# Kernel optimization log

Measured on AMD Instinct MI355X. Metric: run time of the kernel, lower is better.

The kernel has to match this reference:

```python
import jax, jax.numpy as jnp
import numpy as np

N = 100000   # num_rows
M = 50000    # num_cols
D = 32       # embed_dim
E = 5000000  # num observed edges


def setup_inputs() -> dict:
    key = jax.random.key(0)
    ks = jax.random.split(key, 9)
    bound = 1.0 / np.sqrt(D)
    row_embed = jax.random.uniform(ks[0], (N, D), minval=-bound, maxval=bound, dtype=jnp.float32)
    col_embed = jax.random.uniform(ks[1], (M, D), minval=-bound, maxval=bound, dtype=jnp.float32)
    # kaiming_uniform_ with nonlinearity='relu': bound = sqrt(6 / fan_in)
    kb = np.sqrt(6.0 / D)
    W0 = jax.random.uniform(ks[2], (D, D), minval=-kb, maxval=kb, dtype=jnp.float32)
    W1 = jax.random.uniform(ks[3], (D, D), minval=-kb, maxval=kb, dtype=jnp.float32)
    W2 = jax.random.uniform(ks[4], (D, D), minval=-kb, maxval=kb, dtype=jnp.float32)
    b0 = jnp.zeros((D,), jnp.float32)
    b1 = jnp.zeros((D,), jnp.float32)
    b2 = jnp.zeros((D,), jnp.float32)
    edge_index = jax.random.randint(ks[5], (2, E), 0, N + M, dtype=jnp.int64)
    return {"row_embed": row_embed, "col_embed": col_embed,
            "W0": W0, "b0": b0, "W1": W1, "b1": b1, "W2": W2, "b2": b2,
            "edge_index": edge_index}


def reference(row_embed, col_embed, W0, b0, W1, b1, W2, b2, edge_index):
    num_nodes = N + M
    x = jnp.concatenate([row_embed, col_embed], axis=0)  # [N+M, D]
    # add self loops
    loop = jnp.arange(num_nodes, dtype=edge_index.dtype)
    src = jnp.concatenate([edge_index[0], loop])
    dst = jnp.concatenate([edge_index[1], loop])
    for W, b in ((W0, b0), (W1, b1), (W2, b2)):
        h = x @ W.T + b                       # dense linear [N+M, D]
        msg = h[src]                          # gather source features [E+N+M, D]
        agg = jax.ops.segment_sum(msg, dst, num_segments=num_nodes)
        x = jax.nn.relu(agg)
    return (x[:N], x[N:])
```

## Files before the change

kernel.cpp:

```cpp
#include <hip/hip_runtime.h>
#include <hip/hip_fp16.h>

#define N_ROWS 100000
#define NNODES 150000
#define D 32
#define NEDGE 5000000
#define BINSHIFT 7
#define BINSZ 128
#define NBINS 1172
#define NBLK 512
#define SCT 1024
#define CPB ((NEDGE + NBLK - 1) / NBLK)
#define NCOUNTS (NBINS * NBLK)
#define SCAN_ITEMS 1024
#define NSCAN (NCOUNTS / SCAN_ITEMS)

#define LIN_T 128
#define LIN_RPB 256
#define LIN_GRID ((NNODES + LIN_RPB - 1) / LIN_RPB)


__global__ void count_kernel(const int* __restrict__ dst, int* __restrict__ counts) {
    __shared__ int h[4 * NBINS];
    const int t = threadIdx.x;
    const int sub = ((t >> 6) & 3) * NBINS;
    for (int b = t; b < 4 * NBINS; b += SCT) h[b] = 0;
    __syncthreads();
    const int e0 = blockIdx.x * CPB;
    const int e1 = min(e0 + CPB, NEDGE);
    for (int i = e0 + t; i < e1; i += SCT) atomicAdd(&h[sub + (dst[i] >> BINSHIFT)], 1);
    __syncthreads();
    for (int b = t; b < NBINS; b += SCT)
        counts[b * NBLK + blockIdx.x] = h[b] + h[NBINS + b] + h[2 * NBINS + b] + h[3 * NBINS + b];
}


__global__ void scanA(const int* __restrict__ counts, int* __restrict__ partials) {
    __shared__ int s[256];
    const int t = threadIdx.x;
    const int base = blockIdx.x * SCAN_ITEMS + t * 4;
    int sum = 0;
#pragma unroll
    for (int k = 0; k < 4; ++k) sum += counts[base + k];
    s[t] = sum;
    __syncthreads();
    for (int off = 128; off > 0; off >>= 1) {
        if (t < off) s[t] += s[t + off];
        __syncthreads();
    }
    if (t == 0) partials[blockIdx.x] = s[0];
}

__global__ void scanB(int* __restrict__ partials) {
    __shared__ int s[256];
    __shared__ int carry;
    const int t = threadIdx.x;
    if (t == 0) carry = 0;
    __syncthreads();
    for (int c = 0; c < (NSCAN + 255) / 256; ++c) {
        int idx = c * 256 + t;
        int v = (idx < NSCAN) ? partials[idx] : 0;
        s[t] = v;
        __syncthreads();
        for (int off = 1; off < 256; off <<= 1) {
            int tmp = (t >= off) ? s[t - off] : 0;
            __syncthreads();
            s[t] += tmp;
            __syncthreads();
        }
        if (idx < NSCAN) partials[idx] = carry + s[t] - v;
        __syncthreads();
        if (t == 0) carry += s[255];
        __syncthreads();
    }
}

__global__ void scanC(const int* __restrict__ counts, const int* __restrict__ partials,
                      int* __restrict__ bases, int* __restrict__ binPtr) {
    __shared__ int s[256];
    const int t = threadIdx.x;
    const int base = blockIdx.x * SCAN_ITEMS + t * 4;
    int c[4];
    int sum = 0;
#pragma unroll
    for (int k = 0; k < 4; ++k) { c[k] = counts[base + k]; sum += c[k]; }
    s[t] = sum;
    __syncthreads();
    for (int off = 1; off < 256; off <<= 1) {
        int v = (t >= off) ? s[t - off] : 0;
        __syncthreads();
        s[t] += v;
        __syncthreads();
    }
    int run = partials[blockIdx.x] + ((t == 0) ? 0 : s[t - 1]);
#pragma unroll
    for (int k = 0; k < 4; ++k) {
        int idx = base + k;
        bases[idx] = run;
        if ((idx & (NBLK - 1)) == 0) binPtr[idx / NBLK] = run;
        run += c[k];
    }
    if (blockIdx.x == 0 && t == 0) binPtr[NBINS] = NEDGE;
}


__global__ void __launch_bounds__(SCT, 2)
scatter3(const int* __restrict__ src, const int* __restrict__ dst,
         const int* __restrict__ bases, unsigned int* __restrict__ binned) {
    __shared__ int cnt[NBINS];
    __shared__ int lb[NBINS + 1];
    __shared__ int gb[NBINS];
    __shared__ int ssum[SCT];
    __shared__ unsigned int staged[CPB];

    const int t = threadIdx.x;
    const int e0 = blockIdx.x * CPB;
    const int e1 = min(e0 + CPB, NEDGE);
    const int n = e1 - e0;

    for (int b = t; b < NBINS; b += SCT) {
        cnt[b] = 0;
        gb[b] = bases[b * NBLK + blockIdx.x];
    }
    __syncthreads();
    for (int i = e0 + t; i < e1; i += SCT) atomicAdd(&cnt[dst[i] >> BINSHIFT], 1);
    __syncthreads();

    const int i0 = 2 * t, i1 = 2 * t + 1;
    const int c0 = (i0 < NBINS) ? cnt[i0] : 0;
    const int c1 = (i1 < NBINS) ? cnt[i1] : 0;
    ssum[t] = c0 + c1;
    __syncthreads();
    for (int off = 1; off < SCT; off <<= 1) {
        int v = (t >= off) ? ssum[t - off] : 0;
        __syncthreads();
        ssum[t] += v;
        __syncthreads();
    }
    const int excl = (t == 0) ? 0 : ssum[t - 1];
    if (i0 < NBINS) lb[i0] = excl;
    if (i1 < NBINS) lb[i1] = excl + c0;
    if (t == 0) lb[NBINS] = n;
    __syncthreads();

    for (int b = t; b < NBINS; b += SCT) cnt[b] = lb[b];
    __syncthreads();
    for (int i = e0 + t; i < e1; i += SCT) {
        const int dv = dst[i];
        const int bn = dv >> BINSHIFT;
        const int slot = atomicAdd(&cnt[bn], 1);
        staged[slot] = ((unsigned)(dv & (BINSZ - 1)) << 18) | (unsigned)src[i];
    }
    __syncthreads();

    for (int s2 = t; s2 < n; s2 += SCT) {
        int lo = 0, hi = NBINS;
        while (hi - lo > 1) {
            const int mid = (lo + hi) >> 1;
            if (lb[mid] <= s2) lo = mid; else hi = mid;
        }
        binned[gb[lo] + (s2 - lb[lo])] = staged[s2];
    }
}


__global__ void fine_sort(const int* __restrict__ binPtr, const unsigned int* __restrict__ binned,
                          int* __restrict__ rowptr, int* __restrict__ srcSorted) {
    __shared__ int hist[16 * BINSZ];
    __shared__ int cnt[BINSZ];
    __shared__ int rowStart[BINSZ];
    const int t = threadIdx.x;
    const int w = t >> 6;
    const int bin = blockIdx.x;
    const int nodeBase = bin << BINSHIFT;
    const int nNodes = min(BINSZ, NNODES - nodeBase);
    const int e0 = binPtr[bin];
    const int e1 = binPtr[bin + 1];

    for (int i = t; i < 16 * BINSZ; i += 1024) hist[i] = 0;
    __syncthreads();
    for (int e = e0 + t; e < e1; e += 1024)
        atomicAdd(&hist[(w << 7) | (binned[e] >> 18)], 1);
    __syncthreads();
    if (t < BINSZ) {
        int run = 0;
        for (int w2 = 0; w2 < 16; ++w2) {
            const int c = hist[(w2 << 7) | t];
            hist[(w2 << 7) | t] = run;
            run += c;
        }
        cnt[t] = run;
        rowStart[t] = run;
    }
    __syncthreads();
    for (int off = 1; off < BINSZ; off <<= 1) {
        int v = 0;
        if (t < BINSZ && t >= off) v = rowStart[t - off];
        __syncthreads();
        if (t < BINSZ) rowStart[t] += v;
        __syncthreads();
    }
    if (t < nNodes) rowptr[nodeBase + t] = e0 + rowStart[t] - cnt[t];
    for (int i = t; i < 16 * BINSZ; i += 1024) {
        const int r = i & 127;
        hist[i] += rowStart[r] - cnt[r];
    }
    __syncthreads();
    for (int e = e0 + t; e < e1; e += 1024) {
        const unsigned u = binned[e];
        const int r = (int)(u >> 18);
        const int p = atomicAdd(&hist[(w << 7) | r], 1);
        srcSorted[e0 + p] = (int)(u & 0x3FFFFu);
    }
    if (bin == 0 && t == 0) rowptr[NNODES] = NEDGE;
}


template <int MODE>
__global__ void __launch_bounds__(LIN_T)
linear_rows(const float* __restrict__ xa, const float* __restrict__ xb,
            const float* __restrict__ W, const float* __restrict__ b,
            __half* __restrict__ H) {
    __shared__ float xs[LIN_RPB * 33];
    __shared__ float Ws[32 * 36];
    __shared__ float bs[32];
    const int t = threadIdx.x;

    for (int i = t; i < 1024; i += LIN_T) {
        const int c = i >> 5, k = i & 31;
        Ws[k * 36 + c] = W[i];
    }
    if (t < 32) bs[t] = b[t];

    const long long ebase = (long long)blockIdx.x * (LIN_RPB * 32);
#pragma unroll 4
    for (int i = 0; i < (LIN_RPB * 32) / LIN_T; ++i) {
        const long long e = ebase + i * LIN_T + t;
        const int flat = i * LIN_T + t;
        float v = 0.0f;
        if (e < (long long)NNODES * 32) {
            if (MODE == 0) {
                v = (e < (long long)N_ROWS * 32) ? xa[e] : xb[e - (long long)N_ROWS * 32];
            } else {
                v = fmaxf(xa[e], 0.0f);
            }
        }
        xs[(flat >> 5) * 33 + (flat & 31)] = v;
    }
    __syncthreads();

    float a0[32], a1[32];
#pragma unroll
    for (int c = 0; c < 32; ++c) { a0[c] = bs[c]; a1[c] = bs[c]; }
    const int r0 = 2 * t, r1 = 2 * t + 1;
#pragma unroll
    for (int k = 0; k < 32; ++k) {
        const float x0 = xs[r0 * 33 + k];
        const float x1 = xs[r1 * 33 + k];
        const float4* wr = (const float4*)&Ws[k * 36];
#pragma unroll
        for (int q = 0; q < 8; ++q) {
            const float4 w = wr[q];
            a0[4 * q + 0] = fmaf(x0, w.x, a0[4 * q + 0]);
            a0[4 * q + 1] = fmaf(x0, w.y, a0[4 * q + 1]);
            a0[4 * q + 2] = fmaf(x0, w.z, a0[4 * q + 2]);
            a0[4 * q + 3] = fmaf(x0, w.w, a0[4 * q + 3]);
            a1[4 * q + 0] = fmaf(x1, w.x, a1[4 * q + 0]);
            a1[4 * q + 1] = fmaf(x1, w.y, a1[4 * q + 1]);
            a1[4 * q + 2] = fmaf(x1, w.z, a1[4 * q + 2]);
            a1[4 * q + 3] = fmaf(x1, w.w, a1[4 * q + 3]);
        }
    }
    __syncthreads();

    unsigned* os = (unsigned*)xs;
#pragma unroll
    for (int p = 0; p < 16; ++p) {
        __half2 h0 = __floats2half2_rn(a0[2 * p], a0[2 * p + 1]);
        __half2 h1 = __floats2half2_rn(a1[2 * p], a1[2 * p + 1]);
        os[r0 * 17 + p] = *(unsigned*)&h0;
        os[r1 * 17 + p] = *(unsigned*)&h1;
    }
    __syncthreads();
    unsigned* H2 = (unsigned*)H;
    const long long obase = (long long)blockIdx.x * (LIN_RPB * 16);
#pragma unroll 4
    for (int i = 0; i < (LIN_RPB * 16) / LIN_T; ++i) {
        const long long o = obase + i * LIN_T + t;
        const int flat = i * LIN_T + t;
        if (o < (long long)NNODES * 16)
            H2[o] = os[(flat >> 4) * 17 + (flat & 15)];
    }
}


template <bool RELU>
__global__ void agg_csr(const int* __restrict__ rowptr, const int* __restrict__ srcSorted,
                        const __half* __restrict__ H, float* __restrict__ OUT) {
    const int tid = threadIdx.x;
    const int d = blockIdx.x * 16 + (tid >> 4);
    const int j = tid & 15;
    const unsigned int* __restrict__ H2 = (const unsigned int*)H;

    int e = rowptr[d];
    const int eEnd = rowptr[d + 1];
    float2 acc = __half22float2(((const __half2*)H)[d * 16 + j]);
    for (; e + 7 < eEnd; e += 8) {
        int s[8];
#pragma unroll
        for (int k = 0; k < 8; ++k) s[k] = srcSorted[e + k];
        unsigned int v[8];
#pragma unroll
        for (int k = 0; k < 8; ++k) v[k] = H2[s[k] * 16 + j];
#pragma unroll
        for (int k = 0; k < 8; ++k) {
            const float2 f = __half22float2(*(const __half2*)&v[k]);
            acc.x += f.x;
            acc.y += f.y;
        }
    }
    for (; e < eEnd; ++e) {
        const unsigned int v = H2[srcSorted[e] * 16 + j];
        const float2 f = __half22float2(*(const __half2*)&v);
        acc.x += f.x;
        acc.y += f.y;
    }
    if (RELU) { acc.x = fmaxf(acc.x, 0.0f); acc.y = fmaxf(acc.y, 0.0f); }
    ((float2*)OUT)[d * 16 + j] = acc;
}


extern "C" void kernel_launch(void* const* d_in, const int* in_sizes, int n_in,
                              void* d_out, int out_size, void* d_ws, size_t ws_size,
                              hipStream_t stream) {
    const float* row_embed = (const float*)d_in[0];
    const float* col_embed = (const float*)d_in[1];
    const float* W0 = (const float*)d_in[2];
    const float* b0 = (const float*)d_in[3];
    const float* W1 = (const float*)d_in[4];
    const float* b1 = (const float*)d_in[5];
    const float* W2 = (const float*)d_in[6];
    const float* b2 = (const float*)d_in[7];
    const int* ei = (const int*)d_in[8];
    const int* src = ei;
    const int* dst = ei + NEDGE;
    float* out = (float*)d_out;

    __half* H = (__half*)d_ws;
    float* B0 = (float*)(H + (size_t)NNODES * D);
    unsigned int* binned = (unsigned int*)(B0 + (size_t)NNODES * D);
    int* srcSorted = (int*)(binned + NEDGE);
    int* counts = srcSorted + NEDGE;
    int* bases = counts + NCOUNTS;
    int* partials = bases + NCOUNTS;
    int* binPtr = partials + NSCAN;
    int* rowptr = binPtr + (NBINS + 1);

    const int agg_grid = NNODES / 16;

    count_kernel<<<NBLK, SCT, 0, stream>>>(dst, counts);
    scanA<<<NSCAN, 256, 0, stream>>>(counts, partials);
    scanB<<<1, 256, 0, stream>>>(partials);
    scanC<<<NSCAN, 256, 0, stream>>>(counts, partials, bases, binPtr);
    scatter3<<<NBLK, SCT, 0, stream>>>(src, dst, bases, binned);
    fine_sort<<<NBINS, 1024, 0, stream>>>(binPtr, binned, rowptr, srcSorted);

    linear_rows<0><<<LIN_GRID, LIN_T, 0, stream>>>(row_embed, col_embed, W0, b0, H);
    agg_csr<false><<<agg_grid, 256, 0, stream>>>(rowptr, srcSorted, H, B0);
    linear_rows<1><<<LIN_GRID, LIN_T, 0, stream>>>(B0, nullptr, W1, b1, H);
    agg_csr<false><<<agg_grid, 256, 0, stream>>>(rowptr, srcSorted, H, B0);
    linear_rows<1><<<LIN_GRID, LIN_T, 0, stream>>>(B0, nullptr, W2, b2, H);
    agg_csr<true><<<agg_grid, 256, 0, stream>>>(rowptr, srcSorted, H, out);

    (void)in_sizes; (void)n_in; (void)out_size; (void)ws_size;
}
```

Measured before the change: 383.3 us.

## Bucket edges by source range and aggregate source buckets in lockstep per block

Fine sort now orders each destination's edges by one of 8 source-id ranges and emits per-(node,bucket) row pointers into the reused counts buffer. The aggregation kernel has each 16-lane group handle 8 consecutive destinations, and the whole block walks the source buckets in order. The intent is that concurrent gathers from H hit a narrower address range at a time, which should improve L2 locality. In exchange it adds an integer division per edge in the sort, an 8x larger row-pointer array, and more loop overhead with short inner runs in the aggregation.

```diff
diff --git a/kernel.cpp b/kernel.cpp
--- a/kernel.cpp
+++ b/kernel.cpp
@@ -15,6 +15,9 @@
 #define SCAN_ITEMS 1024
 #define NSCAN (NCOUNTS / SCAN_ITEMS)
 
+#define NB 8
+#define BDIV 18750
+
 #define LIN_T 128
 #define LIN_RPB 256
 #define LIN_GRID ((NNODES + LIN_RPB - 1) / LIN_RPB)
@@ -164,55 +167,46 @@
 }
 
 
-__global__ void fine_sort(const int* __restrict__ binPtr, const unsigned int* __restrict__ binned,
-                          int* __restrict__ rowptr, int* __restrict__ srcSorted) {
-    __shared__ int hist[16 * BINSZ];
-    __shared__ int cnt[BINSZ];
-    __shared__ int rowStart[BINSZ];
-    const int t = threadIdx.x;
-    const int w = t >> 6;
+__global__ void fine_sort8(const int* __restrict__ binPtr, const unsigned int* __restrict__ binned,
+                           int* __restrict__ qrowptr, int* __restrict__ srcSorted) {
+    __shared__ int cnt[BINSZ * NB];
+    __shared__ int cur[BINSZ * NB];
+    const int t = threadIdx.x;
     const int bin = blockIdx.x;
-    const int nodeBase = bin << BINSHIFT;
-    const int nNodes = min(BINSZ, NNODES - nodeBase);
     const int e0 = binPtr[bin];
     const int e1 = binPtr[bin + 1];
 
-    for (int i = t; i < 16 * BINSZ; i += 1024) hist[i] = 0;
-    __syncthreads();
-    for (int e = e0 + t; e < e1; e += 1024)
-        atomicAdd(&hist[(w << 7) | (binned[e] >> 18)], 1);
-    __syncthreads();
-    if (t < BINSZ) {
-        int run = 0;
-        for (int w2 = 0; w2 < 16; ++w2) {
-            const int c = hist[(w2 << 7) | t];
-            hist[(w2 << 7) | t] = run;
-            run += c;
-        }
-        cnt[t] = run;
-        rowStart[t] = run;
-    }
-    __syncthreads();
-    for (int off = 1; off < BINSZ; off <<= 1) {
-        int v = 0;
-        if (t < BINSZ && t >= off) v = rowStart[t - off];
-        __syncthreads();
-        if (t < BINSZ) rowStart[t] += v;
-        __syncthreads();
-    }
-    if (t < nNodes) rowptr[nodeBase + t] = e0 + rowStart[t] - cnt[t];
-    for (int i = t; i < 16 * BINSZ; i += 1024) {
-        const int r = i & 127;
-        hist[i] += rowStart[r] - cnt[r];
-    }
+    cnt[t] = 0;
     __syncthreads();
     for (int e = e0 + t; e < e1; e += 1024) {
         const unsigned u = binned[e];
-        const int r = (int)(u >> 18);
-        const int p = atomicAdd(&hist[(w << 7) | r], 1);
-        srcSorted[e0 + p] = (int)(u & 0x3FFFFu);
-    }
-    if (bin == 0 && t == 0) rowptr[NNODES] = NEDGE;
+        const unsigned s = u & 0x3FFFFu;
+        const int key = (int)((u >> 18) * NB) + (int)(s / BDIV);
+        atomicAdd(&cnt[key], 1);
+    }
+    __syncthreads();
+    cur[t] = cnt[t];
+    __syncthreads();
+    for (int off = 1; off < BINSZ * NB; off <<= 1) {
+        int v = (t >= off) ? cur[t - off] : 0;
+        __syncthreads();
+        cur[t] += v;
+        __syncthreads();
+    }
+    {
+        const int excl = cur[t] - cnt[t];
+        qrowptr[bin * (BINSZ * NB) + t] = e0 + excl;
+        cur[t] = excl;
+    }
+    __syncthreads();
+    for (int e = e0 + t; e < e1; e += 1024) {
+        const unsigned u = binned[e];
+        const unsigned s = u & 0x3FFFFu;
+        const int key = (int)((u >> 18) * NB) + (int)(s / BDIV);
+        const int p = atomicAdd(&cur[key], 1);
+        srcSorted[e0 + p] = (int)s;
+    }
+    if (bin == 0 && t == 0) qrowptr[NBINS * (BINSZ * NB)] = NEDGE;
 }
 
 
@@ -295,38 +289,68 @@
 
 
 template <bool RELU>
-__global__ void agg_csr(const int* __restrict__ rowptr, const int* __restrict__ srcSorted,
-                        const __half* __restrict__ H, float* __restrict__ OUT) {
+__global__ void __launch_bounds__(256)
+agg_bkt(const int* __restrict__ qrowptr, const int* __restrict__ srcSorted,
+        const __half* __restrict__ H, float* __restrict__ OUT) {
     const int tid = threadIdx.x;
-    const int d = blockIdx.x * 16 + (tid >> 4);
+    const int g = tid >> 4;
     const int j = tid & 15;
+    const int d0 = blockIdx.x * BINSZ + g * 8;
     const unsigned int* __restrict__ H2 = (const unsigned int*)H;
 
-    int e = rowptr[d];
-    const int eEnd = rowptr[d + 1];
-    float2 acc = __half22float2(((const __half2*)H)[d * 16 + j]);
-    for (; e + 7 < eEnd; e += 8) {
-        int s[8];
-#pragma unroll
-        for (int k = 0; k < 8; ++k) s[k] = srcSorted[e + k];
-        unsigned int v[8];
-#pragma unroll
-        for (int k = 0; k < 8; ++k) v[k] = H2[s[k] * 16 + j];
-#pragma unroll
-        for (int k = 0; k < 8; ++k) {
-            const float2 f = __half22float2(*(const __half2*)&v[k]);
-            acc.x += f.x;
-            acc.y += f.y;
-        }
-    }
-    for (; e < eEnd; ++e) {
-        const unsigned int v = H2[srcSorted[e] * 16 + j];
-        const float2 f = __half22float2(*(const __half2*)&v);
-        acc.x += f.x;
-        acc.y += f.y;
-    }
-    if (RELU) { acc.x = fmaxf(acc.x, 0.0f); acc.y = fmaxf(acc.y, 0.0f); }
-    ((float2*)OUT)[d * 16 + j] = acc;
+    float2 acc[8];
+    int cur[8];
+#pragma unroll
+    for (int r = 0; r < 8; ++r) {
+        const int d = d0 + r;
+        if (d < NNODES) {
+            acc[r] = __half22float2(((const __half2*)H)[d * 16 + j]);
+        } else {
+            acc[r].x = 0.0f; acc[r].y = 0.0f;
+        }
+        cur[r] = qrowptr[d * NB];
+    }
+
+    for (int q = 0; q < NB; ++q) {
+#pragma unroll
+        for (int r = 0; r < 8; ++r) {
+            int e = cur[r];
+            const int eEnd = qrowptr[(d0 + r) * NB + q + 1];
+            for (; e + 3 < eEnd; e += 4) {
+                const int s0 = srcSorted[e];
+                const int s1 = srcSorted[e + 1];
+                const int s2 = srcSorted[e + 2];
+                const int s3 = srcSorted[e + 3];
+                const unsigned v0 = H2[s0 * 16 + j];
+                const unsigned v1 = H2[s1 * 16 + j];
+                const unsigned v2 = H2[s2 * 16 + j];
+                const unsigned v3 = H2[s3 * 16 + j];
+                const float2 f0 = __half22float2(*(const __half2*)&v0);
+                const float2 f1 = __half22float2(*(const __half2*)&v1);
+                const float2 f2 = __half22float2(*(const __half2*)&v2);
+                const float2 f3 = __half22float2(*(const __half2*)&v3);
+                acc[r].x += f0.x + f1.x + f2.x + f3.x;
+                acc[r].y += f0.y + f1.y + f2.y + f3.y;
+            }
+            for (; e < eEnd; ++e) {
+                const unsigned v = H2[srcSorted[e] * 16 + j];
+                const float2 f = __half22float2(*(const __half2*)&v);
+                acc[r].x += f.x;
+                acc[r].y += f.y;
+            }
+            cur[r] = eEnd;
+        }
+    }
+
+#pragma unroll
+    for (int r = 0; r < 8; ++r) {
+        const int d = d0 + r;
+        if (d < NNODES) {
+            float2 o = acc[r];
+            if (RELU) { o.x = fmaxf(o.x, 0.0f); o.y = fmaxf(o.y, 0.0f); }
+            ((float2*)OUT)[d * 16 + j] = o;
+        }
+    }
 }
 
 
@@ -354,23 +378,23 @@
     int* bases = counts + NCOUNTS;
     int* partials = bases + NCOUNTS;
     int* binPtr = partials + NSCAN;
-    int* rowptr = binPtr + (NBINS + 1);
-
-    const int agg_grid = NNODES / 16;
+    int* qrowptr = counts;
+
+    const int agg_grid = NBINS;
 
     count_kernel<<<NBLK, SCT, 0, stream>>>(dst, counts);
     scanA<<<NSCAN, 256, 0, stream>>>(counts, partials);
     scanB<<<1, 256, 0, stream>>>(partials);
     scanC<<<NSCAN, 256, 0, stream>>>(counts, partials, bases, binPtr);
     scatter3<<<NBLK, SCT, 0, stream>>>(src, dst, bases, binned);
-    fine_sort<<<NBINS, 1024, 0, stream>>>(binPtr, binned, rowptr, srcSorted);
+    fine_sort8<<<NBINS, 1024, 0, stream>>>(binPtr, binned, qrowptr, srcSorted);
 
     linear_rows<0><<<LIN_GRID, LIN_T, 0, stream>>>(row_embed, col_embed, W0, b0, H);
-    agg_csr<false><<<agg_grid, 256, 0, stream>>>(rowptr, srcSorted, H, B0);
+    agg_bkt<false><<<agg_grid, 256, 0, stream>>>(qrowptr, srcSorted, H, B0);
     linear_rows<1><<<LIN_GRID, LIN_T, 0, stream>>>(B0, nullptr, W1, b1, H);
-    agg_csr<false><<<agg_grid, 256, 0, stream>>>(rowptr, srcSorted, H, B0);
+    agg_bkt<false><<<agg_grid, 256, 0, stream>>>(qrowptr, srcSorted, H, B0);
     linear_rows<1><<<LIN_GRID, LIN_T, 0, stream>>>(B0, nullptr, W2, b2, H);
-    agg_csr<true><<<agg_grid, 256, 0, stream>>>(rowptr, srcSorted, H, out);
+    agg_bkt<true><<<agg_grid, 256, 0, stream>>>(qrowptr, srcSorted, H, out);
 
     (void)in_sizes; (void)n_in; (void)out_size; (void)ws_size;
 }
```

Result: slower. 696.6 us (+81.7%).

## Sort each destination's edges by source range and copy staged bins per-bin

Applied to the files above, without the earlier changes.

The fine sort now keys edges by destination and by one of eight source-id ranges, so within each destination row the gathered source rows are grouped by range. This is meant to improve cache locality for the H gathers in the three aggregation passes. Scatter3 drops its per-element binary search and copies each bin's staged run with a 16-lane group instead. The per-row pointer array grows eightfold and reuses the counts buffer, which adds scan work and memory traffic in the sort.

```diff
diff --git a/kernel.cpp b/kernel.cpp
--- a/kernel.cpp
+++ b/kernel.cpp
@@ -15,6 +15,9 @@
 #define SCAN_ITEMS 1024
 #define NSCAN (NCOUNTS / SCAN_ITEMS)
 
+#define NB 8
+#define BDIV 18750
+
 #define LIN_T 128
 #define LIN_RPB 256
 #define LIN_GRID ((NNODES + LIN_RPB - 1) / LIN_RPB)
@@ -153,66 +156,58 @@
     }
     __syncthreads();
 
-    for (int s2 = t; s2 < n; s2 += SCT) {
-        int lo = 0, hi = NBINS;
-        while (hi - lo > 1) {
-            const int mid = (lo + hi) >> 1;
-            if (lb[mid] <= s2) lo = mid; else hi = mid;
-        }
-        binned[gb[lo] + (s2 - lb[lo])] = staged[s2];
-    }
-}
-
-
-__global__ void fine_sort(const int* __restrict__ binPtr, const unsigned int* __restrict__ binned,
-                          int* __restrict__ rowptr, int* __restrict__ srcSorted) {
-    __shared__ int hist[16 * BINSZ];
-    __shared__ int cnt[BINSZ];
-    __shared__ int rowStart[BINSZ];
-    const int t = threadIdx.x;
-    const int w = t >> 6;
+    const int grp = t >> 4;
+    const int lane = t & 15;
+    for (int b = grp; b < NBINS; b += 64) {
+        const int lo = lb[b];
+        const int hi = lb[b + 1];
+        const int gbase = gb[b] - lo;
+        for (int s2 = lo + lane; s2 < hi; s2 += 16)
+            binned[gbase + s2] = staged[s2];
+    }
+}
+
+
+__global__ void fine_sort8(const int* __restrict__ binPtr, const unsigned int* __restrict__ binned,
+                           int* __restrict__ qrowptr, int* __restrict__ srcSorted) {
+    __shared__ int cnt[BINSZ * NB];
+    __shared__ int cur[BINSZ * NB];
+    const int t = threadIdx.x;
     const int bin = blockIdx.x;
-    const int nodeBase = bin << BINSHIFT;
-    const int nNodes = min(BINSZ, NNODES - nodeBase);
     const int e0 = binPtr[bin];
     const int e1 = binPtr[bin + 1];
 
-    for (int i = t; i < 16 * BINSZ; i += 1024) hist[i] = 0;
-    __syncthreads();
-    for (int e = e0 + t; e < e1; e += 1024)
-        atomicAdd(&hist[(w << 7) | (binned[e] >> 18)], 1);
-    __syncthreads();
-    if (t < BINSZ) {
-        int run = 0;
-        for (int w2 = 0; w2 < 16; ++w2) {
-            const int c = hist[(w2 << 7) | t];
-            hist[(w2 << 7) | t] = run;
-            run += c;
-        }
-        cnt[t] = run;
-        rowStart[t] = run;
-    }
-    __syncthreads();
-    for (int off = 1; off < BINSZ; off <<= 1) {
-        int v = 0;
-        if (t < BINSZ && t >= off) v = rowStart[t - off];
-        __syncthreads();
-        if (t < BINSZ) rowStart[t] += v;
-        __syncthreads();
-    }
-    if (t < nNodes) rowptr[nodeBase + t] = e0 + rowStart[t] - cnt[t];
-    for (int i = t; i < 16 * BINSZ; i += 1024) {
-        const int r = i & 127;
-        hist[i] += rowStart[r] - cnt[r];
-    }
+    cnt[t] = 0;
     __syncthreads();
     for (int e = e0 + t; e < e1; e += 1024) {
         const unsigned u = binned[e];
-        const int r = (int)(u >> 18);
-        const int p = atomicAdd(&hist[(w << 7) | r], 1);
-        srcSorted[e0 + p] = (int)(u & 0x3FFFFu);
-    }
-    if (bin == 0 && t == 0) rowptr[NNODES] = NEDGE;
+        const unsigned s = u & 0x3FFFFu;
+        const int key = (int)((u >> 18) * NB) + (int)(s / BDIV);
+        atomicAdd(&cnt[key], 1);
+    }
+    __syncthreads();
+    cur[t] = cnt[t];
+    __syncthreads();
+    for (int off = 1; off < BINSZ * NB; off <<= 1) {
+        int v = (t >= off) ? cur[t - off] : 0;
+        __syncthreads();
+        cur[t] += v;
+        __syncthreads();
+    }
+    {
+        const int excl = cur[t] - cnt[t];
+        qrowptr[bin * (BINSZ * NB) + t] = e0 + excl;
+        cur[t] = excl;
+    }
+    __syncthreads();
+    for (int e = e0 + t; e < e1; e += 1024) {
+        const unsigned u = binned[e];
+        const unsigned s = u & 0x3FFFFu;
+        const int key = (int)((u >> 18) * NB) + (int)(s / BDIV);
+        const int p = atomicAdd(&cur[key], 1);
+        srcSorted[e0 + p] = (int)s;
+    }
+    if (bin == 0 && t == 0) qrowptr[NBINS * (BINSZ * NB)] = NEDGE;
 }
 
 
@@ -295,15 +290,15 @@
 
 
 template <bool RELU>
-__global__ void agg_csr(const int* __restrict__ rowptr, const int* __restrict__ srcSorted,
+__global__ void agg_csr(const int* __restrict__ qrowptr, const int* __restrict__ srcSorted,
                         const __half* __restrict__ H, float* __restrict__ OUT) {
     const int tid = threadIdx.x;
     const int d = blockIdx.x * 16 + (tid >> 4);
     const int j = tid & 15;
     const unsigned int* __restrict__ H2 = (const unsigned int*)H;
 
-    int e = rowptr[d];
-    const int eEnd = rowptr[d + 1];
+    int e = qrowptr[d * NB];
+    const int eEnd = qrowptr[d * NB + NB];
     float2 acc = __half22float2(((const __half2*)H)[d * 16 + j]);
     for (; e + 7 < eEnd; e += 8) {
         int s[8];
@@ -354,7 +349,7 @@
     int* bases = counts + NCOUNTS;
     int* partials = bases + NCOUNTS;
     int* binPtr = partials + NSCAN;
-    int* rowptr = binPtr + (NBINS + 1);
+    int* qrowptr = counts;
 
     const int agg_grid = NNODES / 16;
 
@@ -363,14 +358,14 @@
     scanB<<<1, 256, 0, stream>>>(partials);
     scanC<<<NSCAN, 256, 0, stream>>>(counts, partials, bases, binPtr);
     scatter3<<<NBLK, SCT, 0, stream>>>(src, dst, bases, binned);
-    fine_sort<<<NBINS, 1024, 0, stream>>>(binPtr, binned, rowptr, srcSorted);
+    fine_sort8<<<NBINS, 1024, 0, stream>>>(binPtr, binned, qrowptr, srcSorted);
 
     linear_rows<0><<<LIN_GRID, LIN_T, 0, stream>>>(row_embed, col_embed, W0, b0, H);
-    agg_csr<false><<<agg_grid, 256, 0, stream>>>(rowptr, srcSorted, H, B0);
+    agg_csr<false><<<agg_grid, 256, 0, stream>>>(qrowptr, srcSorted, H, B0);
     linear_rows<1><<<LIN_GRID, LIN_T, 0, stream>>>(B0, nullptr, W1, b1, H);
-    agg_csr<false><<<agg_grid, 256, 0, stream>>>(rowptr, srcSorted, H, B0);
+    agg_csr<false><<<agg_grid, 256, 0, stream>>>(qrowptr, srcSorted, H, B0);
     linear_rows<1><<<LIN_GRID, LIN_T, 0, stream>>>(B0, nullptr, W2, b2, H);
-    agg_csr<true><<<agg_grid, 256, 0, stream>>>(rowptr, srcSorted, H, out);
+    agg_csr<true><<<agg_grid, 256, 0, stream>>>(qrowptr, srcSorted, H, out);
 
     (void)in_sizes; (void)n_in; (void)out_size; (void)ws_size;
 }
```

After: 376.4 us. No clear change (-1.8%).
